# Kernel tuning notes

Hardware: AMD Instinct MI355X
Metric: run time of the kernel (lower is better)

The kernel has to match this reference:

```python
import jax, jax.numpy as jnp
import numpy as np

N = 262144          # active voxels
C_IN = 64
C_OUT = 64
BATCH = 2
D0, D1, D2 = 128, 128, 128   # sparse spatial grid
VOL = D0 * D1 * D2


def setup_inputs() -> dict:
    key = jax.random.key(0)
    kf, kw = jax.random.split(key, 2)
    # unique voxel coordinates (submanifold conv assumes no duplicate sites)
    rng = np.random.default_rng(0)
    packed = rng.choice(BATCH * VOL, size=N, replace=False)
    b = packed // VOL
    r = packed % VOL
    i0 = r // (D1 * D2)
    r2 = r % (D1 * D2)
    i1 = r2 // D2
    i2 = r2 % D2
    indices = jnp.asarray(np.stack([b, i0, i1, i2], axis=1), dtype=jnp.int32)  # [N,4]
    features = jax.random.normal(kf, (N, C_IN), dtype=jnp.float32)
    # KRSC layout: [out_ch, k0, k1, k2, in_ch], trunc_normal(std=0.02) ~ normal here
    weight = jax.random.normal(kw, (C_OUT, 3, 3, 3, C_IN), dtype=jnp.float32) * 0.02
    bias = jnp.zeros((C_OUT,), dtype=jnp.float32)
    return {"features": features, "weight": weight, "bias": bias, "indices": indices}


def reference(features, weight, bias, indices):
    n = features.shape[0]
    idx = indices.astype(jnp.int32)
    # linearize (b, i0, i1, i2); packing is linear in coords so neighbor pack = pack + shift
    packed = idx[:, 0] * VOL + idx[:, 1] * (D1 * D2) + idx[:, 2] * D2 + idx[:, 3]
    order = jnp.argsort(packed)
    sorted_pack = packed[order]
    out = jnp.zeros((n, C_OUT), dtype=features.dtype)
    for k0 in range(3):
        for k1 in range(3):
            for k2 in range(3):
                shift = (k0 - 1) * (D1 * D2) + (k1 - 1) * D2 + (k2 - 1)
                neigh_pack = packed + shift
                p = jnp.searchsorted(sorted_pack, neigh_pack)
                pc = jnp.minimum(p, n - 1)
                ok = (p < n) & (sorted_pack[pc] == neigh_pack)
                src = jnp.where(ok, order[pc], 0)
                gathered = jnp.where(ok[:, None], features[src], 0.0)  # [N, C_in]
                out = out + gathered @ weight[:, k0, k1, k2, :].T      # [N, C_out]
    return out + bias
```

## Files before the change

### kernel.cpp

```cpp
#include <hip/hip_runtime.h>

#define VOL   2097152
#define TBL   4194304
#define D1D2  16384
#define DD2   128
#define TILE  128

typedef __bf16 bf16_t;
typedef bf16_t bf16x8 __attribute__((ext_vector_type(8)));
typedef float  floatx4 __attribute__((ext_vector_type(4)));


__global__ __launch_bounds__(256) void prep_k(const float* __restrict__ f,
                                              const float* __restrict__ w,
                                              const int* __restrict__ idx,
                                              int* __restrict__ table,
                                              bf16_t* __restrict__ wb,
                                              bf16_t* __restrict__ fb, int n) {
    const int b = blockIdx.x;
    const int tblB = (n + 255) >> 8;
    if (b < tblB) {
        int t = b * 256 + threadIdx.x;
        if (t < n) {
            int4 c = ((const int4*)idx)[t];
            int p = ((c.x * 128 + c.y) * 128 + c.z) * 128 + c.w;
            table[p] = t;
        }
    } else if (b < tblB + 432) {
        int t = (b - tblB) * 256 + threadIdx.x;
        if (t < 27 * 64 * 64) {
            int ci = t & 63, co = (t >> 6) & 63, k = t >> 12;
            wb[t] = (bf16_t)w[(co * 27 + k) * 64 + ci];
        }
    } else {
        int t = (b - tblB - 432) * 256 + threadIdx.x;
        int pos = t >> 3, c = (t & 7) * 8;
        if (pos < n) {
            const float* src = f + (size_t)pos * 64 + c;
            float4 a  = *(const float4*)src;
            float4 b2 = *(const float4*)(src + 4);
            bf16x8 o = { (bf16_t)a.x,  (bf16_t)a.y,  (bf16_t)a.z,  (bf16_t)a.w,
                         (bf16_t)b2.x, (bf16_t)b2.y, (bf16_t)b2.z, (bf16_t)b2.w };
            *(bf16x8*)(fb + (size_t)pos * 64 + c) = o;
        }
    }
}


__global__ __launch_bounds__(256) void conv_k(
        const bf16_t* __restrict__ fb, const bf16_t* __restrict__ wb,
        const int* __restrict__ table, const int* __restrict__ idx,
        const float* __restrict__ bias, float* __restrict__ out, int n)
{
    __shared__ int    s_pkd[TILE];
    __shared__ int    s_nbr[27 * TILE];
    __shared__ bf16_t sF[TILE * 72];
    __shared__ bf16_t sW[64 * 72];

    const int t    = threadIdx.x;
    const int tile = blockIdx.x * TILE;

    if (t < TILE) {
        int vn = tile + t;
        if (vn < n) {
            int4 c = ((const int4*)idx)[vn];
            s_pkd[t] = ((c.x * 128 + c.y) * 128 + c.z) * 128 + c.w;
        } else {
            s_pkd[t] = (int)0xC0000000;
        }
    }
    __syncthreads();

    for (int u = t; u < 27 * TILE; u += 256) {
        int k  = u >> 7;
        int r  = u & (TILE - 1);
        int k0 = k / 9, k1 = (k / 3) % 3, k2 = k % 3;
        int np = s_pkd[r] + (k0 - 1) * D1D2 + (k1 - 1) * DD2 + (k2 - 1);
        s_nbr[u] = (np >= 0 && np < TBL) ? table[np] : -1;
    }

    const int lane = t & 63;
    const int w    = t >> 6;
    const int l15  = lane & 15;
    const int q    = lane >> 4;

    const int rF = t >> 1;
    const int hF = t & 1;
    const int rW = t >> 2;
    const int cW = t & 3;

    floatx4 acc[8] = {};

    __syncthreads();

    bf16x8 pf[4] = {{}, {}, {}, {}};
    bf16x8 pw0, pw1;
    {
        int nbr = s_nbr[rF];
        if (nbr >= 0) {
            const bf16x8* src = (const bf16x8*)(fb + (size_t)nbr * 64 + hF * 32);
            pf[0] = src[0];
            pf[1] = src[1];
            pf[2] = src[2];
            pf[3] = src[3];
        }
        const bf16x8* wsrc = (const bf16x8*)(wb + rW * 64 + cW * 16);
        pw0 = wsrc[0];
        pw1 = wsrc[1];
    }

    for (int k = 0; k < 27; ++k) {
        *(bf16x8*)&sF[rF * 72 + hF * 32]      = pf[0];
        *(bf16x8*)&sF[rF * 72 + hF * 32 + 8]  = pf[1];
        *(bf16x8*)&sF[rF * 72 + hF * 32 + 16] = pf[2];
        *(bf16x8*)&sF[rF * 72 + hF * 32 + 24] = pf[3];
        *(bf16x8*)&sW[rW * 72 + cW * 16]      = pw0;
        *(bf16x8*)&sW[rW * 72 + cW * 16 + 8]  = pw1;

        if (k + 1 < 27) {
            int nbr = s_nbr[(k + 1) * TILE + rF];
            bf16x8 n0 = {}, n1 = {}, n2 = {}, n3 = {};
            if (nbr >= 0) {
                const bf16x8* src = (const bf16x8*)(fb + (size_t)nbr * 64 + hF * 32);
                n0 = src[0];
                n1 = src[1];
                n2 = src[2];
                n3 = src[3];
            }
            const bf16x8* wsrc = (const bf16x8*)(wb + ((k + 1) * 64 + rW) * 64 + cW * 16);
            pw0   = wsrc[0];
            pw1   = wsrc[1];
            pf[0] = n0;
            pf[1] = n1;
            pf[2] = n2;
            pf[3] = n3;
        }

        __syncthreads();

        #pragma unroll
        for (int s = 0; s < 2; ++s) {
            bf16x8 a = *(const bf16x8*)&sW[(w * 16 + l15) * 72 + s * 32 + q * 8];
            #pragma unroll
            for (int g = 0; g < 8; ++g) {
                bf16x8 bfrag = *(const bf16x8*)&sF[(g * 16 + l15) * 72 + s * 32 + q * 8];
                acc[g] = __builtin_amdgcn_mfma_f32_16x16x32_bf16(a, bfrag, acc[g], 0, 0, 0);
            }
        }

        __syncthreads();
    }

    float4 bs = *(const float4*)&bias[w * 16 + q * 4];
    #pragma unroll
    for (int g = 0; g < 8; ++g) {
        int vn = tile + g * 16 + l15;
        if (vn < n) {
            float4 o;
            o.x = acc[g][0] + bs.x;
            o.y = acc[g][1] + bs.y;
            o.z = acc[g][2] + bs.z;
            o.w = acc[g][3] + bs.w;
            *(float4*)&out[(size_t)vn * 64 + w * 16 + q * 4] = o;
        }
    }
}


extern "C" void kernel_launch(void* const* d_in, const int* in_sizes, int n_in,
                              void* d_out, int out_size, void* d_ws, size_t ws_size,
                              hipStream_t stream) {
    const float* feat = (const float*)d_in[0];
    const float* wgt  = (const float*)d_in[1];
    const float* bias = (const float*)d_in[2];
    const int*   idx  = (const int*)d_in[3];
    float* out = (float*)d_out;

    const int n = in_sizes[0] / 64;

    char* ws = (char*)d_ws;
    int*    table = (int*)ws;
    bf16_t* wbf   = (bf16_t*)(ws + (size_t)TBL * 4);
    bf16_t* fbf   = (bf16_t*)(ws + (size_t)TBL * 4 + 262144);

    hipMemsetAsync(table, 0xFF, (size_t)TBL * 4, stream);

    int tblB = (n + 255) >> 8;
    int fB   = (n * 8 + 255) >> 8;
    prep_k<<<tblB + 432 + fB, 256, 0, stream>>>(feat, wgt, idx, table, wbf, fbf, n);

    conv_k<<<(n + TILE - 1) / TILE, 256, 0, stream>>>(fbf, wbf, table, idx, bias, out, n);
}
```

Before: 239.0 us.

## Sort voxels spatially via table compaction to improve gather locality

Scans the dense hash table with a count/scan/compact pass to get voxels in spatial (packed-coordinate) order. Features are then reordered into bf16 in that order, the table is rewritten to hold sorted positions, and each conv tile processes spatially adjacent voxels, scattering outputs back to their original rows. This makes the 27 neighbor gathers hit nearby rows and improves cache reuse. The cost is three extra kernel launches and two more full passes over the 16 MB table.

```diff
diff --git a/kernel.cpp b/kernel.cpp
--- a/kernel.cpp
+++ b/kernel.cpp
@@ -11,12 +11,10 @@
 typedef float  floatx4 __attribute__((ext_vector_type(4)));
 
 
-__global__ __launch_bounds__(256) void prep_k(const float* __restrict__ f,
-                                              const float* __restrict__ w,
+__global__ __launch_bounds__(256) void prep_k(const float* __restrict__ w,
                                               const int* __restrict__ idx,
                                               int* __restrict__ table,
-                                              bf16_t* __restrict__ wb,
-                                              bf16_t* __restrict__ fb, int n) {
+                                              bf16_t* __restrict__ wb, int n) {
     const int b = blockIdx.x;
     const int tblB = (n + 255) >> 8;
     if (b < tblB) {
@@ -26,33 +24,117 @@
             int p = ((c.x * 128 + c.y) * 128 + c.z) * 128 + c.w;
             table[p] = t;
         }
-    } else if (b < tblB + 432) {
+    } else {
         int t = (b - tblB) * 256 + threadIdx.x;
         if (t < 27 * 64 * 64) {
             int ci = t & 63, co = (t >> 6) & 63, k = t >> 12;
             wb[t] = (bf16_t)w[(co * 27 + k) * 64 + ci];
         }
-    } else {
-        int t = (b - tblB - 432) * 256 + threadIdx.x;
-        int pos = t >> 3, c = (t & 7) * 8;
-        if (pos < n) {
-            const float* src = f + (size_t)pos * 64 + c;
-            float4 a  = *(const float4*)src;
-            float4 b2 = *(const float4*)(src + 4);
-            bf16x8 o = { (bf16_t)a.x,  (bf16_t)a.y,  (bf16_t)a.z,  (bf16_t)a.w,
-                         (bf16_t)b2.x, (bf16_t)b2.y, (bf16_t)b2.z, (bf16_t)b2.w };
-            *(bf16x8*)(fb + (size_t)pos * 64 + c) = o;
-        }
+    }
+}
+
+
+__global__ __launch_bounds__(256) void count_k(const int* __restrict__ table,
+                                               int* __restrict__ rc) {
+    __shared__ int s[256];
+    const int t = threadIdx.x;
+    const int base = blockIdx.x * 4096 + t * 16;
+    int c = 0;
+    #pragma unroll
+    for (int i = 0; i < 4; ++i) {
+        int4 v = ((const int4*)(table + base))[i];
+        c += (v.x >= 0) + (v.y >= 0) + (v.z >= 0) + (v.w >= 0);
+    }
+    s[t] = c;
+    __syncthreads();
+    for (int off = 128; off; off >>= 1) {
+        if (t < off) s[t] += s[t + off];
+        __syncthreads();
+    }
+    if (t == 0) rc[blockIdx.x] = s[0];
+}
+
+__global__ __launch_bounds__(1024) void scan_k(const int* __restrict__ rc,
+                                               int* __restrict__ rb) {
+    __shared__ int s[1024];
+    const int t = threadIdx.x;
+    int v = rc[t];
+    s[t] = v;
+    __syncthreads();
+    int x = v;
+    for (int off = 1; off < 1024; off <<= 1) {
+        int y = (t >= off) ? s[t - off] : 0;
+        __syncthreads();
+        x += y;
+        s[t] = x;
+        __syncthreads();
+    }
+    rb[t] = x - v;
+}
+
+__global__ __launch_bounds__(256) void compact_k(int* __restrict__ table,
+                                                 int* __restrict__ ord,
+                                                 int* __restrict__ pkd,
+                                                 const int* __restrict__ rb) {
+    __shared__ int s_cnt[256];
+    const int t = threadIdx.x;
+    const int base = blockIdx.x * 4096 + t * 16;
+
+    int v[16];
+    #pragma unroll
+    for (int i = 0; i < 4; ++i)
+        *(int4*)&v[i * 4] = ((const int4*)(table + base))[i];
+    int cnt = 0;
+    #pragma unroll
+    for (int i = 0; i < 16; ++i) cnt += (v[i] >= 0);
+
+    s_cnt[t] = cnt;
+    __syncthreads();
+    int x = cnt;
+    for (int off = 1; off < 256; off <<= 1) {
+        int y = (t >= off) ? s_cnt[t - off] : 0;
+        __syncthreads();
+        x += y;
+        s_cnt[t] = x;
+        __syncthreads();
+    }
+
+    int pos = rb[blockIdx.x] + x - cnt;
+    #pragma unroll
+    for (int i = 0; i < 16; ++i) {
+        if (v[i] >= 0) {
+            ord[pos] = v[i];
+            pkd[pos] = base + i;
+            table[base + i] = pos;
+            ++pos;
+        }
+    }
+}
+
+__global__ void feat_k(const float* __restrict__ f, const int* __restrict__ ord,
+                       bf16_t* __restrict__ fbp, int n) {
+    int t = blockIdx.x * blockDim.x + threadIdx.x;
+    int pos = t >> 3, c = (t & 7) * 8;
+    if (pos < n) {
+        int orig = ord[pos];
+        const float* src = f + (size_t)orig * 64 + c;
+        float4 a  = *(const float4*)src;
+        float4 b2 = *(const float4*)(src + 4);
+        bf16x8 o = { (bf16_t)a.x,  (bf16_t)a.y,  (bf16_t)a.z,  (bf16_t)a.w,
+                     (bf16_t)b2.x, (bf16_t)b2.y, (bf16_t)b2.z, (bf16_t)b2.w };
+        *(bf16x8*)(fbp + (size_t)pos * 64 + c) = o;
     }
 }
 
 
 __global__ __launch_bounds__(256) void conv_k(
-        const bf16_t* __restrict__ fb, const bf16_t* __restrict__ wb,
-        const int* __restrict__ table, const int* __restrict__ idx,
-        const float* __restrict__ bias, float* __restrict__ out, int n)
+        const bf16_t* __restrict__ fbp, const bf16_t* __restrict__ wb,
+        const int* __restrict__ table, const int* __restrict__ pkd,
+        const int* __restrict__ ord, const float* __restrict__ bias,
+        float* __restrict__ out, int n)
 {
     __shared__ int    s_pkd[TILE];
+    __shared__ int    s_ord[TILE];
     __shared__ int    s_nbr[27 * TILE];
     __shared__ bf16_t sF[TILE * 72];
     __shared__ bf16_t sW[64 * 72];
@@ -62,12 +144,8 @@
 
     if (t < TILE) {
         int vn = tile + t;
-        if (vn < n) {
-            int4 c = ((const int4*)idx)[vn];
-            s_pkd[t] = ((c.x * 128 + c.y) * 128 + c.z) * 128 + c.w;
-        } else {
-            s_pkd[t] = (int)0xC0000000;
-        }
+        s_pkd[t] = (vn < n) ? pkd[vn] : (int)0xC0000000;
+        s_ord[t] = (vn < n) ? ord[vn] : 0;
     }
     __syncthreads();
 
@@ -98,7 +176,7 @@
     {
         int nbr = s_nbr[rF];
         if (nbr >= 0) {
-            const bf16x8* src = (const bf16x8*)(fb + (size_t)nbr * 64 + hF * 32);
+            const bf16x8* src = (const bf16x8*)(fbp + (size_t)nbr * 64 + hF * 32);
             pf[0] = src[0];
             pf[1] = src[1];
             pf[2] = src[2];
@@ -121,7 +199,7 @@
             int nbr = s_nbr[(k + 1) * TILE + rF];
             bf16x8 n0 = {}, n1 = {}, n2 = {}, n3 = {};
             if (nbr >= 0) {
-                const bf16x8* src = (const bf16x8*)(fb + (size_t)nbr * 64 + hF * 32);
+                const bf16x8* src = (const bf16x8*)(fbp + (size_t)nbr * 64 + hF * 32);
                 n0 = src[0];
                 n1 = src[1];
                 n2 = src[2];
@@ -156,12 +234,13 @@
     for (int g = 0; g < 8; ++g) {
         int vn = tile + g * 16 + l15;
         if (vn < n) {
+            int orig = s_ord[g * 16 + l15];
             float4 o;
             o.x = acc[g][0] + bs.x;
             o.y = acc[g][1] + bs.y;
             o.z = acc[g][2] + bs.z;
             o.w = acc[g][3] + bs.w;
-            *(float4*)&out[(size_t)vn * 64 + w * 16 + q * 4] = o;
+            *(float4*)&out[(size_t)orig * 64 + w * 16 + q * 4] = o;
         }
     }
 }
@@ -181,13 +260,22 @@
     char* ws = (char*)d_ws;
     int*    table = (int*)ws;
     bf16_t* wbf   = (bf16_t*)(ws + (size_t)TBL * 4);
-    bf16_t* fbf   = (bf16_t*)(ws + (size_t)TBL * 4 + 262144);
+    bf16_t* fbp   = (bf16_t*)(ws + (size_t)TBL * 4 + 262144);
+    int*    ord   = (int*)(ws + (size_t)TBL * 4 + 262144 + (size_t)n * 128);
+    int*    pkd   = ord + n;
+    int*    rc    = pkd + n;
+    int*    rb    = rc + 1024;
 
     hipMemsetAsync(table, 0xFF, (size_t)TBL * 4, stream);
 
     int tblB = (n + 255) >> 8;
-    int fB   = (n * 8 + 255) >> 8;
-    prep_k<<<tblB + 432 + fB, 256, 0, stream>>>(feat, wgt, idx, table, wbf, fbf, n);
-
-    conv_k<<<(n + TILE - 1) / TILE, 256, 0, stream>>>(fbf, wbf, table, idx, bias, out, n);
-}
+    prep_k<<<tblB + 432, 256, 0, stream>>>(wgt, idx, table, wbf, n);
+    count_k<<<1024, 256, 0, stream>>>(table, rc);
+    scan_k<<<1, 1024, 0, stream>>>(rc, rb);
+    compact_k<<<1024, 256, 0, stream>>>(table, ord, pkd, rb);
+
+    int nu = n * 8;
+    feat_k<<<(nu + 255) / 256, 256, 0, stream>>>(feat, ord, fbp, n);
+
+    conv_k<<<(n + TILE - 1) / TILE, 256, 0, stream>>>(fbp, wbf, table, pkd, ord, bias, out, n);
+}
```

New measurement: 244.9 us. 1.02x slower.
